# Kernel optimization log

Measured on AMD Instinct MI355X. Metric: run time of the kernel, lower is better.

Reference implementation:

```python
import jax, jax.numpy as jnp
import numpy as np
import math

B, L, HID = 2, 1024, 1536
NH, HD = 24, 64
DSSM = NH * HD            # 1536 (expand = 1)
QKV = 3 * DSSM
DCONV = 2
EPS = 1e-6


def _silu(u):
    return u * jax.nn.sigmoid(u)


def setup_inputs() -> dict:
    key = jax.random.key(0)
    ks = jax.random.split(key, 10)
    x = jax.random.normal(ks[0], (B, L, HID), dtype=jnp.float32)
    w_qkv = jax.random.normal(ks[1], (QKV, HID), dtype=jnp.float32) / math.sqrt(HID)
    conv_w = jax.random.normal(ks[2], (QKV, DCONV), dtype=jnp.float32) * 0.5  # depthwise causal conv, k=2
    w_dt = jax.random.normal(ks[3], (NH, HID), dtype=jnp.float32) * 0.02
    # dt_bias init exactly as in the torch module
    dt = jnp.exp(jax.random.uniform(ks[4], (NH,)) * (math.log(0.1) - math.log(0.001)) + math.log(0.001))
    dt = jnp.clip(dt, 1e-4, None)
    dt_bias = dt + jnp.log(-jnp.expm1(-dt))
    a_log = jnp.log(jax.random.uniform(ks[5], (NH,), minval=1.0, maxval=16.0))
    D = jnp.ones((NH, HD), dtype=jnp.float32)
    w_z = jax.random.normal(ks[6], (DSSM, HID), dtype=jnp.float32) / math.sqrt(HID)
    b_z = jnp.zeros((DSSM,), dtype=jnp.float32)
    rms_w = jnp.ones((DSSM,), dtype=jnp.float32)
    w_o = jax.random.normal(ks[7], (HID, DSSM), dtype=jnp.float32) / math.sqrt(DSSM)
    return dict(x=x, w_qkv=w_qkv, conv_w=conv_w, w_dt=w_dt, dt_bias=dt_bias,
                a_log=a_log, D=D, w_z=w_z, b_z=b_z, rms_w=rms_w, w_o=w_o)


def reference(x, w_qkv, conv_w, w_dt, dt_bias, a_log, D, w_z, b_z, rms_w, w_o):
    # qkv projection  [B,L,3*DSSM]
    qkv = jnp.einsum('blh,qh->blq', x, w_qkv)
    # depthwise causal conv1d (kernel size 2, padding k-1, trimmed to L)
    prev = jnp.pad(qkv, ((0, 0), (1, 0), (0, 0)))[:, :L]
    qkv = _silu(prev * conv_w[:, 0] + qkv * conv_w[:, 1])
    q, k, v = jnp.split(qkv, 3, axis=-1)
    q = q.reshape(B, L, NH, HD)
    k = k.reshape(B, L, NH, HD)
    v = v.reshape(B, L, NH, HD)
    # dt discretization: softplus(dt_proj(x) + dt_bias)   [B,L,NH]
    dt = jax.nn.softplus(jnp.einsum('blh,nh->bln', x, w_dt) + dt_bias)
    A = -jnp.exp(a_log)              # [NH], negative
    dA = dt * A                      # [B,L,NH]
    cs = jnp.transpose(jnp.cumsum(dA, axis=1), (0, 2, 1))   # [B,NH,L]
    diff = cs[:, :, :, None] - cs[:, :, None, :]            # [B,NH,L,L], <=0 on causal part
    causal = jnp.tril(jnp.ones((L, L), dtype=bool))
    decay = jnp.exp(jnp.where(causal, diff, -jnp.inf))      # segment-sum decay matrix
    # quadratic SSD (attention) form of the selective scan
    scores = jnp.einsum('bihd,bjhd->bhij', q, k) * decay
    scores = scores * jnp.transpose(dt, (0, 2, 1))[:, :, None, :]  # dt_j on keys (B-discretization)
    y = jnp.einsum('bhij,bjhd->bihd', scores, v)
    y = y + v * D                    # D skip connection
    y = y.reshape(B, L, DSSM)
    # z gate + RMSNorm + output projection
    z = jnp.einsum('blh,dh->bld', x, w_z) + b_z
    y = y * _silu(z)
    y = y * jax.lax.rsqrt(jnp.mean(y * y, axis=-1, keepdims=True) + EPS) * rms_w
    return jnp.einsum('bld,hd->blh', y, w_o)
```

## Files before the change

kernel.cpp:

```cpp
#include <hip/hip_runtime.h>
#include <hip/hip_bf16.h>
#include <math.h>

#define B_ 2
#define L_ 1024
#define HID_ 1536
#define NH_ 24
#define HD_ 64
#define DSSM_ 1536
#define QKV_ 4608
#define M_ 2048

typedef __attribute__((ext_vector_type(8))) short short8;
typedef __attribute__((ext_vector_type(4))) short short4e;
typedef __attribute__((ext_vector_type(4))) float floatx4;

__device__ __forceinline__ void gload_lds16(const short* g, short* l)
{
    __builtin_amdgcn_global_load_lds(
        (const __attribute__((address_space(1))) void*)g,
        (__attribute__((address_space(3))) void*)l,
        16, 0, 0);
}

__device__ __forceinline__ float bfs2f(short s)
{
    unsigned u = ((unsigned)(unsigned short)s) << 16;
    float f; __builtin_memcpy(&f, &u, 4); return f;
}
__device__ __forceinline__ short f2bfs(float f)
{
    __hip_bfloat16 h = __float2bfloat16(f);
    short s; __builtin_memcpy(&s, &h, 2); return s;
}

__device__ const int pIt[15] = {0,1,2,3,3,4,4,5,5,6,6,6,7,7,7};
__device__ const int pJ0[15] = {0,0,0,0,6,0,6,0,6,0,6,12,0,6,12};
__device__ const int pSl[15] = {0,0,0,0,1,0,1,0,1,0,1,2,0,1,2};

#define CN1 (QKV_ * HID_)
#define CN2 (DSSM_ * HID_)
#define CN3 (HID_ * DSSM_)

#define MFMA_ __builtin_amdgcn_mfma_f32_16x16x32_bf16
#define BAR_() __builtin_amdgcn_s_barrier()
#define SCHED_ __builtin_amdgcn_sched_barrier(0)

__global__ void cast_w_kernel(
    const float* __restrict__ wq,
    const float* __restrict__ wz, const float* __restrict__ wo,
    __hip_bfloat16* __restrict__ wcat,
    __hip_bfloat16* __restrict__ wob)
{
    int i = (blockIdx.x * 256 + threadIdx.x) * 4;
    const float* src; __hip_bfloat16* dst; int off;
    if (i < CN1)             { src = wq; dst = wcat;       off = i; }
    else if (i < CN1 + CN2)  { src = wz; dst = wcat + CN1; off = i - CN1; }
    else                     { src = wo; dst = wob;        off = i - CN1 - CN2; }
    float4 f = *reinterpret_cast<const float4*>(src + off);
    dst[off]     = __float2bfloat16(f.x);
    dst[off + 1] = __float2bfloat16(f.y);
    dst[off + 2] = __float2bfloat16(f.z);
    dst[off + 3] = __float2bfloat16(f.w);
}

__global__ __launch_bounds__(256) void dtproj_kernel(
    const float* __restrict__ x,
    const float* __restrict__ w_dt,
    const float* __restrict__ dt_bias,
    const float* __restrict__ a_log,
    float* __restrict__ dt,
    float* __restrict__ dA,
    __hip_bfloat16* __restrict__ xb)
{
    const int tid  = threadIdx.x;
    const int wave = tid >> 6;
    const int lane = tid & 63;
    const int m0   = blockIdx.x * 8 + wave * 2;

    float4 xa[2][6];
#pragma unroll
    for (int rr = 0; rr < 2; ++rr)
#pragma unroll
        for (int j = 0; j < 6; ++j)
            xa[rr][j] = *reinterpret_cast<const float4*>(
                x + (size_t)(m0 + rr) * HID_ + lane * 4 + j * 256);

    short* xbp = reinterpret_cast<short*>(xb);
#pragma unroll
    for (int rr = 0; rr < 2; ++rr)
#pragma unroll
        for (int j = 0; j < 6; ++j) {
            short4e ov;
            ov[0] = f2bfs(xa[rr][j].x); ov[1] = f2bfs(xa[rr][j].y);
            ov[2] = f2bfs(xa[rr][j].z); ov[3] = f2bfs(xa[rr][j].w);
            *reinterpret_cast<short4e*>(
                xbp + (size_t)(m0 + rr) * HID_ + lane * 4 + j * 256) = ov;
        }

    float acc0[NH_], acc1[NH_];
#pragma unroll
    for (int n = 0; n < NH_; ++n) {
        float s0 = 0.f, s1 = 0.f;
#pragma unroll
        for (int j = 0; j < 6; ++j) {
            float4 w = *reinterpret_cast<const float4*>(
                w_dt + (size_t)n * HID_ + lane * 4 + j * 256);
            s0 += xa[0][j].x * w.x + xa[0][j].y * w.y
                + xa[0][j].z * w.z + xa[0][j].w * w.w;
            s1 += xa[1][j].x * w.x + xa[1][j].y * w.y
                + xa[1][j].z * w.z + xa[1][j].w * w.w;
        }
        acc0[n] = s0;
        acc1[n] = s1;
    }

#pragma unroll
    for (int off = 32; off; off >>= 1) {
#pragma unroll
        for (int n = 0; n < NH_; ++n) {
            acc0[n] += __shfl_xor(acc0[n], off, 64);
            acc1[n] += __shfl_xor(acc1[n], off, 64);
        }
    }

    if (lane < NH_) {
        const int n = lane;
        float bias = dt_bias[n];
        float Aval = -__expf(a_log[n]);
        float v0 = acc0[n] + bias;
        float v1 = acc1[n] + bias;
        v0 = (v0 > 20.f) ? v0 : log1pf(__expf(v0));
        v1 = (v1 > 20.f) ? v1 : log1pf(__expf(v1));
        int b0 = m0 / L_, l0 = m0 % L_;
        size_t o0 = ((size_t)b0 * NH_ + n) * L_ + l0;
        dt[o0]     = v0;
        dA[o0]     = v0 * Aval;
        dt[o0 + 1] = v1;
        dA[o0 + 1] = v1 * Aval;
    }
}

#define CSTR 200

__global__ __launch_bounds__(256, 2) void gemm_qkvz_128(
    const __hip_bfloat16* __restrict__ A,
    const __hip_bfloat16* __restrict__ Bm,
    __hip_bfloat16* __restrict__ qkv_out,
    float* __restrict__ z_out,
    const float* __restrict__ b_z)
{
    extern __shared__ short lds[];
    const int K  = HID_;
    const int NT = K / 64;
    const int tid   = threadIdx.x;
    const int lane  = tid & 63;
    const int wave  = tid >> 6;
    const int col16 = lane & 15;
    const int quad  = lane >> 4;
    const int wm = wave >> 1;
    const int wn = wave & 1;
    const int rowblk = blockIdx.y * 128;
    const int colblk = blockIdx.x * 192;

    const short* Ap = reinterpret_cast<const short*>(A);
    const short* Bp = reinterpret_cast<const short*>(Bm);

    const int o  = tid * 16;
    const int s  = o ^ (((o >> 7) & 7) << 4);
    const int sr = s >> 7;
    const int sc = (s & 127) >> 1;

    const int mask = (col16 & 7) << 4;
    const int e0 = ((quad * 16)      ^ mask) >> 1;
    const int e1 = ((64 + quad * 16) ^ mask) >> 1;
    const int arow = (wm * 64 + col16) * 64;
    const int brow = (wn * 96 + col16) * 64;

    floatx4 acc[4][6] = {};

    auto STAGE_ALL = [&](int c, int t) {
        const short* ga = Ap + (size_t)(rowblk + sr) * K + t * 64 + sc;
        short* da = &lds[c * 8192 + tid * 8];
#pragma unroll
        for (int u = 0; u < 4; ++u)
            gload_lds16(ga + (size_t)(u * 32) * K, da + u * 2048);
        const short* gb = Bp + (size_t)(colblk + sr) * K + t * 64 + sc;
        short* db = &lds[16384 + c * 12288 + tid * 8];
#pragma unroll
        for (int u = 0; u < 6; ++u)
            gload_lds16(gb + (size_t)(u * 32) * K, db + u * 2048);
    };

    STAGE_ALL(0, 0);
    asm volatile("s_waitcnt vmcnt(0)" ::: "memory");
    SCHED_;
    BAR_();

    for (int t = 0; t < NT; ++t) {
        const int cur = t & 1;
        if (t + 1 < NT) STAGE_ALL(cur ^ 1, t + 1);

        const int Ab = cur * 8192;
        const int Bb = 16384 + cur * 12288;
        short8 af0[4], af1[4], bf0[6], bf1[6];
#pragma unroll
        for (int m = 0; m < 4; ++m) {
            af0[m] = *reinterpret_cast<const short8*>(&lds[Ab + arow + m * 1024 + e0]);
            af1[m] = *reinterpret_cast<const short8*>(&lds[Ab + arow + m * 1024 + e1]);
        }
#pragma unroll
        for (int n = 0; n < 6; ++n) {
            bf0[n] = *reinterpret_cast<const short8*>(&lds[Bb + brow + n * 1024 + e0]);
            bf1[n] = *reinterpret_cast<const short8*>(&lds[Bb + brow + n * 1024 + e1]);
        }
        asm volatile("s_waitcnt lgkmcnt(0)" ::: "memory");
        SCHED_;

        __builtin_amdgcn_s_setprio(1);
#pragma unroll
        for (int m = 0; m < 4; ++m)
#pragma unroll
            for (int n = 0; n < 6; ++n) {
                acc[m][n] = MFMA_(af0[m], bf0[n], acc[m][n], 0, 0, 0);
                acc[m][n] = MFMA_(af1[m], bf1[n], acc[m][n], 0, 0, 0);
            }
        __builtin_amdgcn_s_setprio(0);

        asm volatile("s_waitcnt vmcnt(0)" ::: "memory");
        SCHED_;
        BAR_();
    }

    if (blockIdx.x < 24) {
        const int rb = wm * 64 + quad * 4;
        const int cb = wn * 96 + col16;
#pragma unroll
        for (int m = 0; m < 4; ++m)
#pragma unroll
            for (int n = 0; n < 6; ++n)
#pragma unroll
                for (int r = 0; r < 4; ++r)
                    lds[(rb + m * 16 + r) * CSTR + cb + n * 16] =
                        f2bfs(acc[m][n][r]);
        __syncthreads();
        const int row = tid >> 1;
        const int seg = tid & 1;
        const short* srcp = &lds[row * CSTR + seg * 96];
        short* dstp = reinterpret_cast<short*>(qkv_out)
                    + (size_t)(rowblk + row) * QKV_ + colblk + seg * 96;
#pragma unroll
        for (int j = 0; j < 12; ++j)
            *reinterpret_cast<short8*>(dstp + j * 8) =
                *reinterpret_cast<const short8*>(srcp + j * 8);
    } else {
        const int row0  = rowblk + wm * 64;
        const int col0g = colblk + wn * 96 - QKV_;
#pragma unroll
        for (int m = 0; m < 4; ++m)
#pragma unroll
            for (int n = 0; n < 6; ++n)
#pragma unroll
                for (int r = 0; r < 4; ++r) {
                    int row = row0 + m * 16 + quad * 4 + r;
                    int col = col0g + n * 16 + col16;
                    z_out[(size_t)row * DSSM_ + col] = acc[m][n][r] + b_z[col];
                }
    }
}

template<int OUTMODE>
__global__ __launch_bounds__(256) void gemm_nt(
    const __hip_bfloat16* __restrict__ A,
    const __hip_bfloat16* __restrict__ Bm,
    void* __restrict__ Cv,
    const float* __restrict__ bias,
    int M, int N, int K)
{
    const int lane  = threadIdx.x & 63;
    const int wave  = threadIdx.x >> 6;
    const int col16 = lane & 15;
    const int quad  = lane >> 4;
    const int wr    = wave >> 1;
    const int wc    = wave & 1;
    const int rowblk = blockIdx.y * 128;
    const int colblk = blockIdx.x * 128;

    const short* Ap = reinterpret_cast<const short*>(A);
    const short* Bp = reinterpret_cast<const short*>(Bm);

    __shared__ alignas(16) short As[128 * 32];
    __shared__ alignas(16) short Bs[128 * 32];

    const int srow = lane >> 2;
    const int scol = (lane & 3) * 8;

    floatx4 acc[4][4] = {};

    for (int k0 = 0; k0 < K; k0 += 32) {
#pragma unroll
        for (int s2 = 0; s2 < 2; ++s2) {
            const int seg = wave * 2 + s2;
            gload_lds16(Ap + (size_t)(rowblk + seg * 16 + srow) * K + k0 + scol,
                        &As[seg * 512]);
            gload_lds16(Bp + (size_t)(colblk + seg * 16 + srow) * K + k0 + scol,
                        &Bs[seg * 512]);
        }
        __syncthreads();

        short8 af[4], bf[4];
#pragma unroll
        for (int t = 0; t < 4; ++t) {
            af[t] = *reinterpret_cast<const short8*>(
                &As[(wr * 64 + t * 16 + col16) * 32 + quad * 8]);
            bf[t] = *reinterpret_cast<const short8*>(
                &Bs[(wc * 64 + t * 16 + col16) * 32 + quad * 8]);
        }
#pragma unroll
        for (int mt = 0; mt < 4; ++mt)
#pragma unroll
            for (int nt = 0; nt < 4; ++nt)
                acc[mt][nt] = __builtin_amdgcn_mfma_f32_16x16x32_bf16(
                    af[mt], bf[nt], acc[mt][nt], 0, 0, 0);
        __syncthreads();
    }

    const int row0 = rowblk + wr * 64;
    const int col0 = colblk + wc * 64;
#pragma unroll
    for (int mt = 0; mt < 4; ++mt) {
#pragma unroll
        for (int nt = 0; nt < 4; ++nt) {
#pragma unroll
            for (int r = 0; r < 4; ++r) {
                int row = row0 + mt * 16 + quad * 4 + r;
                int col = col0 + nt * 16 + col16;
                float v = acc[mt][nt][r];
                if (OUTMODE == 1) v += bias[col];
                if (OUTMODE == 2)
                    ((__hip_bfloat16*)Cv)[(size_t)row * N + col] = __float2bfloat16(v);
                else
                    ((float*)Cv)[(size_t)row * N + col] = v;
            }
        }
    }
}

#define QK2 (2 * DSSM_)

__global__ __launch_bounds__(256) void convvdt_kernel(
    const __hip_bfloat16* __restrict__ raw,
    const float* __restrict__ conv_w,
    const float* __restrict__ dt,
    const float* __restrict__ dA,
    __hip_bfloat16* __restrict__ q,
    __hip_bfloat16* __restrict__ k,
    __hip_bfloat16* __restrict__ v,
    __hip_bfloat16* __restrict__ vt,
    float* __restrict__ cs)
{
    __shared__ short T[64][72];
    __shared__ float red4[4];
    const int tid = threadIdx.x;

    if (blockIdx.x >= 3840) {
        const int bnh  = blockIdx.x - 3840;
        const int lane = tid & 63;
        const int wave = tid >> 6;
        float4 dv = *reinterpret_cast<const float4*>(dA + (size_t)bnh * L_ + tid * 4);
        float s1 = dv.x + dv.y;
        float s2 = s1 + dv.z;
        float s3 = s2 + dv.w;
        float tot = s3;
        float sc = tot;
#pragma unroll
        for (int off = 1; off < 64; off <<= 1) {
            float o2 = __shfl_up(sc, off, 64);
            if (lane >= off) sc += o2;
        }
        if (lane == 63) red4[wave] = sc;
        __syncthreads();
        float woff = 0.f;
#pragma unroll
        for (int w = 0; w < 4; ++w)
            if (w < wave) woff += red4[w];
        float base = woff + sc - tot;
        float* dst = cs + (size_t)bnh * L_ + tid * 4;
        dst[0] = base + dv.x;
        dst[1] = base + s1;
        dst[2] = base + s2;
        dst[3] = base + s3;
        return;
    }

    if (blockIdx.x < 3072) {
        int idx8 = blockIdx.x * 256 + tid;
        int c8 = (idx8 % (QK2 / 8)) * 8;
        int ml = idx8 / (QK2 / 8);
        int l  = ml % L_;
        int b  = ml / L_;

        const short* base = reinterpret_cast<const short*>(raw) + (size_t)ml * QKV_ + c8;
        short8 curv = *reinterpret_cast<const short8*>(base);
        short8 prevv = {};
        if (l > 0) prevv = *reinterpret_cast<const short8*>(base - QKV_);

        float4 w0 = *reinterpret_cast<const float4*>(conv_w + c8 * 2);
        float4 w1 = *reinterpret_cast<const float4*>(conv_w + c8 * 2 + 4);
        float4 w2 = *reinterpret_cast<const float4*>(conv_w + c8 * 2 + 8);
        float4 w3 = *reinterpret_cast<const float4*>(conv_w + c8 * 2 + 12);
        const float wa[16] = {w0.x, w0.y, w0.z, w0.w, w1.x, w1.y, w1.z, w1.w,
                              w2.x, w2.y, w2.z, w2.w, w3.x, w3.y, w3.z, w3.w};

        short8 outv;
#pragma unroll
        for (int j = 0; j < 8; ++j) {
            float u = bfs2f(prevv[j]) * wa[2 * j] + bfs2f(curv[j]) * wa[2 * j + 1];
            u = fmaxf(u, -80.f);
            outv[j] = f2bfs(u / (1.f + __expf(-u)));
        }

        int part = c8 / DSSM_;
        int cc   = c8 % DSSM_;
        int nh   = cc >> 6;
        int d    = cc & 63;
        __hip_bfloat16* dst = (part == 0) ? q : k;
        *reinterpret_cast<short8*>(
            reinterpret_cast<short*>(dst) + (((size_t)b * NH_ + nh) * L_ + l) * HD_ + d)
            = outv;
        return;
    }

    const int bid2 = blockIdx.x - 3072;
    const int lt0 = (bid2 & 15) * 64;
    const int nh  = (bid2 >> 4) % NH_;
    const int b   = bid2 / (16 * NH_);
    const int bnh = b * NH_ + nh;

    {
        int row = tid >> 2;
        int cc  = (tid & 3) * 16;
        int l   = lt0 + row;
        int cglob = QK2 + nh * 64 + cc;
        const short* rp = reinterpret_cast<const short*>(raw)
                        + (size_t)(b * L_ + l) * QKV_ + cglob;
        short8 cur0 = *reinterpret_cast<const short8*>(rp);
        short8 cur1 = *reinterpret_cast<const short8*>(rp + 8);
        short8 pv0 = {}, pv1 = {};
        if (l > 0) {
            pv0 = *reinterpret_cast<const short8*>(rp - QKV_);
            pv1 = *reinterpret_cast<const short8*>(rp + 8 - QKV_);
        }
        float wa[32];
#pragma unroll
        for (int w4 = 0; w4 < 8; ++w4) {
            float4 wv = *reinterpret_cast<const float4*>(conv_w + cglob * 2 + w4 * 4);
            wa[w4 * 4]     = wv.x; wa[w4 * 4 + 1] = wv.y;
            wa[w4 * 4 + 2] = wv.z; wa[w4 * 4 + 3] = wv.w;
        }
        float dtr = dt[(size_t)bnh * L_ + l];

        short8 vo0, vo1;
#pragma unroll
        for (int j = 0; j < 8; ++j) {
            float u = bfs2f(pv0[j]) * wa[2 * j] + bfs2f(cur0[j]) * wa[2 * j + 1];
            u = fmaxf(u, -80.f);
            float sV = u / (1.f + __expf(-u));
            vo0[j] = f2bfs(sV);
            T[row][cc + j] = f2bfs(sV * dtr);

            float u2 = bfs2f(pv1[j]) * wa[16 + 2 * j] + bfs2f(cur1[j]) * wa[16 + 2 * j + 1];
            u2 = fmaxf(u2, -80.f);
            float sV2 = u2 / (1.f + __expf(-u2));
            vo1[j] = f2bfs(sV2);
            T[row][cc + 8 + j] = f2bfs(sV2 * dtr);
        }
        short* vp = reinterpret_cast<short*>(v)
                  + ((size_t)bnh * L_ + l) * HD_ + cc;
        *reinterpret_cast<short8*>(vp)     = vo0;
        *reinterpret_cast<short8*>(vp + 8) = vo1;
    }
    __syncthreads();
    {
        int d  = tid >> 2;
        int lc = (tid & 3) * 16;
        short8 o0, o1;
#pragma unroll
        for (int j = 0; j < 8; ++j) {
            o0[j] = T[lc + j][d];
            o1[j] = T[lc + 8 + j][d];
        }
        short* dst = reinterpret_cast<short*>(vt)
                   + ((size_t)bnh * HD_ + d) * L_ + lt0 + lc;
        *reinterpret_cast<short8*>(dst)     = o0;
        *reinterpret_cast<short8*>(dst + 8) = o1;
    }
}

__global__ __launch_bounds__(256) void attn_kernel(
    const __hip_bfloat16* __restrict__ q,
    const __hip_bfloat16* __restrict__ k,
    const __hip_bfloat16* __restrict__ vt,
    const float* __restrict__ cs,
    float* __restrict__ p0,
    float* __restrict__ p1,
    float* __restrict__ p2)
{
    const int bid  = blockIdx.x;
    const int xcd  = bid & 7;
    const int tq   = bid >> 3;
    const int g    = (tq / 15) * 8 + xcd;
    const int pidx = tq % 15;
    const int it   = pIt[pidx];
    const int sl   = pSl[pidx];
    const int jt_beg = pJ0[pidx];
    const int b    = g / NH_;
    const int nh   = g % NH_;
    const int tid  = threadIdx.x;
    const int lane = tid & 63;
    const int wave = tid >> 6;
    const int col  = lane & 15;
    const int quad = lane >> 4;
    const int bnh  = b * NH_ + nh;
    const int iw0  = it * 128 + wave * 16;
    const int iw1  = iw0 + 64;

    float* pout = (sl == 0) ? p0 : ((sl == 1) ? p1 : p2);

    const short* qp  = reinterpret_cast<const short*>(q);
    const short* kp  = reinterpret_cast<const short*>(k);
    const short* vtp = reinterpret_cast<const short*>(vt);

    __shared__ alignas(16) short Ks[4096];
    __shared__ alignas(16) short Ps[4 * 2 * 16 * 72];
    __shared__ float Cj[384];

    const int jbase = jt_beg * 64;
    const int jlim  = min(384, L_ - jbase);
    if (tid < (jlim >> 2))
        *reinterpret_cast<float4*>(&Cj[tid * 4]) =
            *reinterpret_cast<const float4*>(cs + (size_t)bnh * L_ + jbase + tid * 4);

    const short* qrow0 = qp + ((size_t)bnh * L_ + iw0 + col) * HD_;
    const short* qrow1 = qp + ((size_t)bnh * L_ + iw1 + col) * HD_;
    short8 aq0_0 = *reinterpret_cast<const short8*>(qrow0 + quad * 8);
    short8 aq0_1 = *reinterpret_cast<const short8*>(qrow0 + 32 + quad * 8);
    short8 aq1_0 = *reinterpret_cast<const short8*>(qrow1 + quad * 8);
    short8 aq1_1 = *reinterpret_cast<const short8*>(qrow1 + 32 + quad * 8);

    float csr0[4], csr1[4];
#pragma unroll
    for (int r = 0; r < 4; ++r) {
        csr0[r] = cs[(size_t)bnh * L_ + iw0 + quad * 4 + r];
        csr1[r] = cs[(size_t)bnh * L_ + iw1 + quad * 4 + r];
    }

    auto STAGE_K = [&](int jt2) {
        const short* gk = kp + ((size_t)bnh * L_ + jt2 * 64 + wave * 16 + (lane >> 2)) * HD_
                        + (lane & 3) * 8;
        gload_lds16(gk,      &Ks[wave * 512 + lane * 8]);
        gload_lds16(gk + 32, &Ks[2048 + wave * 512 + lane * 8]);
    };

    const int jt_end = min(jt_beg + 5, 2 * it + 1);

    STAGE_K(jt_beg);

    floatx4 accO0[4] = {};
    floatx4 accO1[4] = {};

    for (int jt = jt_beg; jt <= jt_end; ++jt) {
        const int j0 = jt * 64;

        asm volatile("s_waitcnt vmcnt(0)" ::: "memory");
        SCHED_;
        __syncthreads();

        short8 bv[2][4];
#pragma unroll
        for (int c = 0; c < 2; ++c) {
            if (j0 + c * 32 <= iw1 + 15) {
#pragma unroll
                for (int nt = 0; nt < 4; ++nt)
                    bv[c][nt] = *reinterpret_cast<const short8*>(
                        vtp + ((size_t)bnh * HD_ + nt * 16 + col) * L_
                            + j0 + c * 32 + quad * 8);
            }
        }

#pragma unroll
        for (int s = 0; s < 4; ++s) {
            int jsub = j0 + s * 16;
            short8 bk0 = *reinterpret_cast<const short8*>(
                &Ks[(s * 16 + col) * 32 + quad * 8]);
            short8 bk1 = *reinterpret_cast<const short8*>(
                &Ks[2048 + (s * 16 + col) * 32 + quad * 8]);
            int j = jsub + col;
            float csj = Cj[j - jbase];

            if (jsub <= iw0 + 15) {
                floatx4 sc = {};
                sc = __builtin_amdgcn_mfma_f32_16x16x32_bf16(aq0_0, bk0, sc, 0, 0, 0);
                sc = __builtin_amdgcn_mfma_f32_16x16x32_bf16(aq0_1, bk1, sc, 0, 0, 0);
#pragma unroll
                for (int r = 0; r < 4; ++r) {
                    int i = iw0 + quad * 4 + r;
                    float e = (j <= i) ? __expf(csr0[r] - csj) : 0.f;
                    Ps[wave * 2304 + (quad * 4 + r) * 72 + s * 16 + col] =
                        f2bfs(sc[r] * e);
                }
            } else if (j0 + (s >> 1) * 32 <= iw0 + 15) {
#pragma unroll
                for (int r = 0; r < 4; ++r)
                    Ps[wave * 2304 + (quad * 4 + r) * 72 + s * 16 + col] = 0;
            }

            if (jsub <= iw1 + 15) {
                floatx4 sc = {};
                sc = __builtin_amdgcn_mfma_f32_16x16x32_bf16(aq1_0, bk0, sc, 0, 0, 0);
                sc = __builtin_amdgcn_mfma_f32_16x16x32_bf16(aq1_1, bk1, sc, 0, 0, 0);
#pragma unroll
                for (int r = 0; r < 4; ++r) {
                    int i = iw1 + quad * 4 + r;
                    float e = (j <= i) ? __expf(csr1[r] - csj) : 0.f;
                    Ps[wave * 2304 + 1152 + (quad * 4 + r) * 72 + s * 16 + col] =
                        f2bfs(sc[r] * e);
                }
            } else if (j0 + (s >> 1) * 32 <= iw1 + 15) {
#pragma unroll
                for (int r = 0; r < 4; ++r)
                    Ps[wave * 2304 + 1152 + (quad * 4 + r) * 72 + s * 16 + col] = 0;
            }
        }

#pragma unroll
        for (int c = 0; c < 2; ++c) {
            if (j0 + c * 32 <= iw0 + 15) {
                short8 pa = *reinterpret_cast<const short8*>(
                    &Ps[wave * 2304 + col * 72 + c * 32 + quad * 8]);
#pragma unroll
                for (int nt = 0; nt < 4; ++nt)
                    accO0[nt] = __builtin_amdgcn_mfma_f32_16x16x32_bf16(
                        pa, bv[c][nt], accO0[nt], 0, 0, 0);
            }
            if (j0 + c * 32 <= iw1 + 15) {
                short8 pa = *reinterpret_cast<const short8*>(
                    &Ps[wave * 2304 + 1152 + col * 72 + c * 32 + quad * 8]);
#pragma unroll
                for (int nt = 0; nt < 4; ++nt)
                    accO1[nt] = __builtin_amdgcn_mfma_f32_16x16x32_bf16(
                        pa, bv[c][nt], accO1[nt], 0, 0, 0);
            }
        }

        __syncthreads();
        if (jt < jt_end) STAGE_K(jt + 1);
    }

#pragma unroll
    for (int nt = 0; nt < 4; ++nt) {
#pragma unroll
        for (int r = 0; r < 4; ++r) {
            int dv = nt * 16 + col;
            int i0 = iw0 + quad * 4 + r;
            int i1 = iw1 + quad * 4 + r;
            pout[((size_t)b * L_ + i0) * DSSM_ + nh * HD_ + dv] = accO0[nt][r];
            pout[((size_t)b * L_ + i1) * DSSM_ + nh * HD_ + dv] = accO1[nt][r];
        }
    }
}

__global__ __launch_bounds__(256) void gate_rms_kernel(
    const float* __restrict__ p0,
    const float* __restrict__ p1,
    const float* __restrict__ p2,
    const float* __restrict__ z,
    const __hip_bfloat16* __restrict__ v,
    const float* __restrict__ Dm,
    const float* __restrict__ rms_w,
    __hip_bfloat16* __restrict__ yn)
{
    int m   = blockIdx.x;
    int b   = m / L_;
    int l   = m % L_;
    int tid = threadIdx.x;
    size_t base = (size_t)m * DSSM_;
    const bool has1 = (l >= 384);
    const bool has2 = (l >= 768);

    floatx4 acc4[2] = {};
    float ss = 0.f;
#pragma unroll
    for (int t = 0; t < 2; ++t) {
        int i4 = t * 256 + tid;
        if (i4 < DSSM_ / 4) {
            int c  = i4 * 4;
            int nh = c >> 6, d = c & 63;
            floatx4 p = *reinterpret_cast<const floatx4*>(p0 + base + c);
            if (has1) p += *reinterpret_cast<const floatx4*>(p1 + base + c);
            if (has2) p += *reinterpret_cast<const floatx4*>(p2 + base + c);
            floatx4 dm = *reinterpret_cast<const floatx4*>(Dm + c);
            floatx4 zz = *reinterpret_cast<const floatx4*>(z + base + c);
            short4e vv = *reinterpret_cast<const short4e*>(
                reinterpret_cast<const short*>(v)
                + (((size_t)b * NH_ + nh) * L_ + l) * HD_ + d);
            floatx4 g;
#pragma unroll
            for (int j = 0; j < 4; ++j) {
                float yv = p[j] + bfs2f(vv[j]) * dm[j];
                float zv = fmaxf(zz[j], -80.f);
                float gv = yv * (zv / (1.f + __expf(-zv)));
                ss += gv * gv;
                g[j] = gv;
            }
            acc4[t] = g;
        }
    }
#pragma unroll
    for (int off = 32; off; off >>= 1) ss += __shfl_xor(ss, off, 64);
    __shared__ float red[4];
    if ((tid & 63) == 0) red[tid >> 6] = ss;
    __syncthreads();
    ss = red[0] + red[1] + red[2] + red[3];
    float r = rsqrtf(ss / (float)DSSM_ + 1e-6f);
#pragma unroll
    for (int t = 0; t < 2; ++t) {
        int i4 = t * 256 + tid;
        if (i4 < DSSM_ / 4) {
            int c = i4 * 4;
            floatx4 rw = *reinterpret_cast<const floatx4*>(rms_w + c);
            short4e o;
#pragma unroll
            for (int j = 0; j < 4; ++j)
                o[j] = f2bfs(acc4[t][j] * r * rw[j]);
            *reinterpret_cast<short4e*>(
                reinterpret_cast<short*>(yn) + base + c) = o;
        }
    }
}

extern "C" void kernel_launch(void* const* d_in, const int* in_sizes, int n_in,
                              void* d_out, int out_size, void* d_ws, size_t ws_size,
                              hipStream_t stream)
{
    const float* x       = (const float*)d_in[0];
    const float* w_qkv   = (const float*)d_in[1];
    const float* conv_w  = (const float*)d_in[2];
    const float* w_dt    = (const float*)d_in[3];
    const float* dt_bias = (const float*)d_in[4];
    const float* a_log   = (const float*)d_in[5];
    const float* Dm      = (const float*)d_in[6];
    const float* w_z     = (const float*)d_in[7];
    const float* b_z     = (const float*)d_in[8];
    const float* rms_w   = (const float*)d_in[9];
    const float* w_o     = (const float*)d_in[10];
    float* out = (float*)d_out;

    char* ws = (char*)d_ws;

    __hip_bfloat16* xb    = (__hip_bfloat16*)(ws);
    __hip_bfloat16* wob   = (__hip_bfloat16*)(ws + 6291456);
    float*          zbuf  = (float*)(ws + 11010048);
    __hip_bfloat16* wcat  = (__hip_bfloat16*)(ws + 23592960);
    __hip_bfloat16* qkvb  = (__hip_bfloat16*)(ws + 42467328);
    __hip_bfloat16* qb    = (__hip_bfloat16*)(ws + 61341696);
    __hip_bfloat16* kb    = (__hip_bfloat16*)(ws + 67633152);
    __hip_bfloat16* vb    = (__hip_bfloat16*)(ws + 73924608);
    float* dt   = (float*)(ws + 80216064);
    float* dA   = (float*)(ws + 80412672);
    float* cs   = (float*)(ws + 80609280);
    __hip_bfloat16* vtb = (__hip_bfloat16*)(ws);
    __hip_bfloat16* yn  = (__hip_bfloat16*)(ws);
    float* p0 = (float*)(ws + 23592960);
    float* p1 = (float*)(ws + 36175872);
    float* p2 = (float*)(ws + 48758784);

    static bool attr_set = false;
    if (!attr_set) {
        (void)hipFuncSetAttribute(reinterpret_cast<const void*>(gemm_qkvz_128),
                                  hipFuncAttributeMaxDynamicSharedMemorySize,
                                  81920);
        attr_set = true;
    }

    cast_w_kernel<<<(CN1 + CN2 + CN3) / 1024, 256, 0, stream>>>(
        w_qkv, w_z, w_o, wcat, wob);

    dtproj_kernel<<<M_ / 8, 256, 0, stream>>>(
        x, w_dt, dt_bias, a_log, dt, dA, xb);

    gemm_qkvz_128<<<dim3((QKV_ + DSSM_) / 192, M_ / 128), 256, 81920, stream>>>(
        xb, wcat, qkvb, zbuf, b_z);

    convvdt_kernel<<<3888, 256, 0, stream>>>(
        qkvb, conv_w, dt, dA, qb, kb, vb, vtb, cs);

    attn_kernel<<<720, 256, 0, stream>>>(
        qb, kb, vtb, cs, p0, p1, p2);

    gate_rms_kernel<<<M_, 256, 0, stream>>>(p0, p1, p2, zbuf, vb, Dm, rms_w, yn);

    gemm_nt<0><<<dim3(HID_ / 128, M_ / 128), 256, 0, stream>>>(
        yn, wob, (void*)out, nullptr, M_, HID_, DSSM_);
}
```

Baseline: 253.1 us.

## Stage K in 128-row chunks and prefetch V ahead of barrier

```diff
diff --git a/kernel.cpp b/kernel.cpp
--- a/kernel.cpp
+++ b/kernel.cpp
@@ -531,7 +531,7 @@
     const short* kp  = reinterpret_cast<const short*>(k);
     const short* vtp = reinterpret_cast<const short*>(vt);
 
-    __shared__ alignas(16) short Ks[4096];
+    __shared__ alignas(16) short Ks[8192];
     __shared__ alignas(16) short Ps[4 * 2 * 16 * 72];
     __shared__ float Cj[384];
 
@@ -555,46 +555,31 @@
         csr1[r] = cs[(size_t)bnh * L_ + iw1 + quad * 4 + r];
     }
 
-    auto STAGE_K = [&](int jt2) {
-        const short* gk = kp + ((size_t)bnh * L_ + jt2 * 64 + wave * 16 + (lane >> 2)) * HD_
-                        + (lane & 3) * 8;
-        gload_lds16(gk,      &Ks[wave * 512 + lane * 8]);
-        gload_lds16(gk + 32, &Ks[2048 + wave * 512 + lane * 8]);
+    auto STAGE_K128 = [&](int t128) {
+        const short* gk = kp + ((size_t)bnh * L_ + jbase + t128 * 128
+                                + wave * 32 + (lane >> 2)) * HD_ + (lane & 3) * 8;
+        gload_lds16(gk,                 &Ks[wave * 1024 + lane * 8]);
+        gload_lds16(gk + 16 * HD_,      &Ks[wave * 1024 + 512 + lane * 8]);
+        gload_lds16(gk + 32,            &Ks[4096 + wave * 1024 + lane * 8]);
+        gload_lds16(gk + 16 * HD_ + 32, &Ks[4096 + wave * 1024 + 512 + lane * 8]);
     };
 
     const int jt_end = min(jt_beg + 5, 2 * it + 1);
-
-    STAGE_K(jt_beg);
+    const int n128 = (jt_end - jt_beg + 1) >> 1;
+
+    STAGE_K128(0);
 
     floatx4 accO0[4] = {};
     floatx4 accO1[4] = {};
 
-    for (int jt = jt_beg; jt <= jt_end; ++jt) {
-        const int j0 = jt * 64;
-
-        asm volatile("s_waitcnt vmcnt(0)" ::: "memory");
-        SCHED_;
-        __syncthreads();
-
-        short8 bv[2][4];
-#pragma unroll
-        for (int c = 0; c < 2; ++c) {
-            if (j0 + c * 32 <= iw1 + 15) {
-#pragma unroll
-                for (int nt = 0; nt < 4; ++nt)
-                    bv[c][nt] = *reinterpret_cast<const short8*>(
-                        vtp + ((size_t)bnh * HD_ + nt * 16 + col) * L_
-                            + j0 + c * 32 + quad * 8);
-            }
-        }
-
+    auto PROCESS = [&](int j0, int h, short8 (&bv)[2][4]) {
 #pragma unroll
         for (int s = 0; s < 4; ++s) {
             int jsub = j0 + s * 16;
             short8 bk0 = *reinterpret_cast<const short8*>(
-                &Ks[(s * 16 + col) * 32 + quad * 8]);
+                &Ks[(h * 64 + s * 16 + col) * 32 + quad * 8]);
             short8 bk1 = *reinterpret_cast<const short8*>(
-                &Ks[2048 + (s * 16 + col) * 32 + quad * 8]);
+                &Ks[4096 + (h * 64 + s * 16 + col) * 32 + quad * 8]);
             int j = jsub + col;
             float csj = Cj[j - jbase];
 
@@ -652,9 +637,45 @@
                         pa, bv[c][nt], accO1[nt], 0, 0, 0);
             }
         }
-
+    };
+
+    for (int t = 0; t < n128; ++t) {
+        const int j0A = jbase + t * 128;
+        const int j0B = j0A + 64;
+
+        short8 bvA[2][4];
+#pragma unroll
+        for (int c = 0; c < 2; ++c) {
+            if (j0A + c * 32 <= iw1 + 15) {
+#pragma unroll
+                for (int nt = 0; nt < 4; ++nt)
+                    bvA[c][nt] = *reinterpret_cast<const short8*>(
+                        vtp + ((size_t)bnh * HD_ + nt * 16 + col) * L_
+                            + j0A + c * 32 + quad * 8);
+            }
+        }
+
+        asm volatile("s_waitcnt vmcnt(0)" ::: "memory");
+        SCHED_;
         __syncthreads();
-        if (jt < jt_end) STAGE_K(jt + 1);
+
+        short8 bvB[2][4];
+#pragma unroll
+        for (int c = 0; c < 2; ++c) {
+            if (j0B + c * 32 <= iw1 + 15) {
+#pragma unroll
+                for (int nt = 0; nt < 4; ++nt)
+                    bvB[c][nt] = *reinterpret_cast<const short8*>(
+                        vtp + ((size_t)bnh * HD_ + nt * 16 + col) * L_
+                            + j0B + c * 32 + quad * 8);
+            }
+        }
+
+        PROCESS(j0A, 0, bvA);
+        PROCESS(j0B, 1, bvB);
+
+        __syncthreads();
+        if (t + 1 < n128) STAGE_K128(t + 1);
     }
 
 #pragma unroll
```

Result: no change. 253.4 us (+0.1%).
